# Kernel optimization log

Hardware: AMD Instinct MI355X
Metric: run time of the kernel (lower is better)

The kernel has to match this reference:

```python
import jax, jax.numpy as jnp
import numpy as np
from jax import lax

B, CHI, CHO, H, W = 8, 128, 128, 64, 64
K = 3
KK = K * K


def setup_inputs() -> dict:
    key = jax.random.key(0)
    ks = jax.random.split(key, 7)
    x = jax.random.normal(ks[0], (B, CHI, H, W), jnp.float32)
    # small offset-conv weights so sampled offsets stay in a realistic few-pixel range
    off_w = jax.random.normal(ks[1], (3 * KK, CHI, K, K), jnp.float32) * 0.01
    off_b = jnp.zeros((3 * KK,), jnp.float32)
    w = jax.random.normal(ks[2], (CHO, CHI, K, K), jnp.float32) / np.sqrt(CHI * KK).astype(np.float32)
    b = jnp.zeros((CHO,), jnp.float32)
    gamma = jax.random.uniform(ks[3], (CHO,), jnp.float32)  # nn.init.uniform_ on BN weight
    beta = jnp.zeros((CHO,), jnp.float32)
    return {"x": x, "off_w": off_w, "off_b": off_b, "w": w, "b": b, "gamma": gamma, "beta": beta}


def _deform_conv(x, off_w, off_b, w, b):
    """DCNv2 modulated deformable conv, k=3, stride=1, pad=1, dil=1, 1 deform group."""
    B_, C, H_, W_ = x.shape
    # offset/mask branch: plain 3x3 conv -> 27 channels (2*9 offsets, 9 masks)
    om = lax.conv_general_dilated(x, off_w, (1, 1), ((1, 1), (1, 1)),
                                  dimension_numbers=("NCHW", "OIHW", "NCHW"))
    om = om + off_b[None, :, None, None]
    off = om[:, : 2 * KK].reshape(B_, KK, 2, H_, W_)  # [B,9,2,H,W]; ch 2k=y, 2k+1=x
    mask = jax.nn.sigmoid(om[:, 2 * KK:])             # [B,9,H,W]

    ky, kx = jnp.meshgrid(jnp.arange(K, dtype=jnp.float32),
                          jnp.arange(K, dtype=jnp.float32), indexing="ij")
    ky = ky.reshape(KK); kx = kx.reshape(KK)
    # sampling positions: p = p0 - pad + k*dil + offset
    py = off[:, :, 0] + (jnp.arange(H_, dtype=jnp.float32) - 1.0)[None, None, :, None] + ky[None, :, None, None]
    px = off[:, :, 1] + (jnp.arange(W_, dtype=jnp.float32) - 1.0)[None, None, None, :] + kx[None, :, None, None]

    y0 = jnp.floor(py); x0 = jnp.floor(px)
    ly = py - y0; lx = px - x0
    xf = x.reshape(B_, C, H_ * W_)

    def corner(yi, xi, wgt):
        valid = ((yi >= 0) & (yi <= H_ - 1) & (xi >= 0) & (xi <= W_ - 1)).astype(x.dtype)
        yc = jnp.clip(yi, 0, H_ - 1).astype(jnp.int32)
        xc = jnp.clip(xi, 0, W_ - 1).astype(jnp.int32)
        idx = (yc * W_ + xc).reshape(B_, KK * H_ * W_)
        g = jax.vmap(lambda xb, ib: xb[:, ib])(xf, idx).reshape(B_, C, KK, H_, W_)
        return g * (valid * wgt)[:, None]

    val = (corner(y0, x0, (1 - ly) * (1 - lx))
           + corner(y0, x0 + 1, (1 - ly) * lx)
           + corner(y0 + 1, x0, ly * (1 - lx))
           + corner(y0 + 1, x0 + 1, ly * lx))  # [B,C,9,H,W]
    val = val * mask[:, None]  # modulation
    out = jnp.einsum("bckhw,ock->bohw", val, w.reshape(w.shape[0], C, KK))
    return out + b[None, :, None, None]


def reference(x, off_w, off_b, w, b, gamma, beta):
    y = _deform_conv(x, off_w, off_b, w, b)
    # BatchNorm2d in training mode (batch statistics), eps=1e-5, then ReLU
    mean = y.mean(axis=(0, 2, 3))
    var = y.var(axis=(0, 2, 3))
    yn = (y - mean[None, :, None, None]) * lax.rsqrt(var[None, :, None, None] + 1e-5)
    return jax.nn.relu(yn * gamma[None, :, None, None] + beta[None, :, None, None])
```

## Files before the change

### kernel.cpp

```cpp
#include <hip/hip_runtime.h>
#include <hip/hip_bf16.h>
#include <math.h>

#define B_ 8
#define HH 64
#define WW 64
#define HW 4096
#define LDV 136

typedef __bf16 bf16x8 __attribute__((ext_vector_type(8)));
typedef float floatx4 __attribute__((ext_vector_type(4)));
typedef unsigned int uint4a __attribute__((ext_vector_type(4)));

#define WS_Y    0u
#define WS_SC   16777216u
#define WS_SH   16778240u
#define WS_XTB  16779264u
#define WS_WTB  25167872u
#define WS_OWB  25462784u

static __device__ inline ushort f2bf(float f) {
  __hip_bfloat16 h = __float2bfloat16(f);
  return __builtin_bit_cast(ushort, h);
}
static __device__ inline float lo16(unsigned int u) { return __builtin_bit_cast(float, u << 16); }
static __device__ inline float hi16(unsigned int u) { return __builtin_bit_cast(float, u & 0xffff0000u); }

__global__ __launch_bounds__(256) void k_prepw(const float* __restrict__ w,
                                               const float* __restrict__ ow,
                                               ushort* __restrict__ wtb,
                                               ushort* __restrict__ owb) {
  int idx = blockIdx.x * 256 + threadIdx.x;
  if (idx < 147456) {
    int c = idx & 127, o = (idx >> 7) & 127, k = idx >> 14;
    wtb[idx] = f2bf(w[(o * 128 + c) * 9 + k]);
  } else {
    int j = idx - 147456;
    if (j < 36864) {
      int c = j & 127, o = (j >> 7) & 31, k = j >> 12;
      float v = (o < 27) ? ow[(o * 128 + c) * 9 + k] : 0.f;
      owb[j] = f2bf(v);
    }
  }
}

__global__ __launch_bounds__(256) void k_xt(const float* __restrict__ x,
                                            ushort* __restrict__ xtb) {
  __shared__ float tile[32][33];
  int hw0 = blockIdx.x * 32;
  int c0 = blockIdx.y * 32;
  int b = blockIdx.z;
  int col = threadIdx.x & 31, row = threadIdx.x >> 5;
  const float* xb = x + ((size_t)b * 128 + c0) * HW + hw0;
#pragma unroll
  for (int i = 0; i < 32; i += 8)
    tile[row + i][col] = xb[(size_t)(row + i) * HW + col];
  __syncthreads();
  int cpair = threadIdx.x & 15, hwi = threadIdx.x >> 4;
  ushort* xo = xtb + ((size_t)b * HW + hw0) * 128 + c0;
#pragma unroll
  for (int i = 0; i < 32; i += 16) {
    int hw = hwi + i;
    unsigned int v = (unsigned int)f2bf(tile[2 * cpair][hw]) |
                     ((unsigned int)f2bf(tile[2 * cpair + 1][hw]) << 16);
    *(unsigned int*)(&xo[(size_t)hw * 128 + 2 * cpair]) = v;
  }
}

__global__ __launch_bounds__(256) void k_main(
    const ushort* __restrict__ xtb, const ushort* __restrict__ wtb,
    const ushort* __restrict__ owb, const float* __restrict__ off_b,
    const float* __restrict__ bias, float* __restrict__ y) {
  __shared__ ushort Vl[64 * LDV];
  __shared__ float omL[27 * 64];
  int t = threadIdx.x;
  int lane = t & 63, wv = t >> 6;
  int li = lane & 15, quad = lane >> 4;
  int row = blockIdx.x, b = blockIdx.y;
  const ushort* xb = xtb + (size_t)b * HW * 128;
  int sp = lane, scg = wv;

  floatx4 oacc[2];
  oacc[0] = (floatx4){0.f, 0.f, 0.f, 0.f};
  oacc[1] = (floatx4){0.f, 0.f, 0.f, 0.f};
  for (int k = 0; k < 9; ++k) {
    int ky = k / 3, kx = k % 3;
    int ry = row - 1 + ky;
    int col = sp - 1 + kx;
    bool v = (ry >= 0 && ry < HH && col >= 0 && col < WW);
    const uint4a* src = (const uint4a*)(xb + ((size_t)(ry * WW + col) * 128 + scg * 32));
    __syncthreads();
#pragma unroll
    for (int j = 0; j < 4; ++j) {
      uint4a d = (uint4a){0u, 0u, 0u, 0u};
      if (v) d = src[j];
      *(uint4a*)(&Vl[sp * LDV + scg * 32 + j * 8]) = d;
    }
    __syncthreads();
#pragma unroll
    for (int ks = 0; ks < 4; ++ks) {
      bf16x8 bfrag = __builtin_bit_cast(bf16x8,
          *(const uint4a*)(&Vl[(wv * 16 + li) * LDV + ks * 32 + quad * 8]));
#pragma unroll
      for (int ot = 0; ot < 2; ++ot) {
        bf16x8 afrag = __builtin_bit_cast(bf16x8,
            *(const uint4a*)(&owb[(size_t)(k * 32 + ot * 16 + li) * 128 + ks * 32 + quad * 8]));
        oacc[ot] = __builtin_amdgcn_mfma_f32_16x16x32_bf16(afrag, bfrag, oacc[ot], 0, 0, 0);
      }
    }
  }
  __syncthreads();
#pragma unroll
  for (int ot = 0; ot < 2; ++ot)
#pragma unroll
    for (int r = 0; r < 4; ++r) {
      int o = ot * 16 + quad * 4 + r;
      if (o < 27) omL[o * 64 + wv * 16 + li] = oacc[ot][r] + off_b[o];
    }
  __syncthreads();

  int oh = wv & 1, ph = wv >> 1;
  floatx4 macc[4][2];
#pragma unroll
  for (int i = 0; i < 4; ++i) {
    macc[i][0] = (floatx4){0.f, 0.f, 0.f, 0.f};
    macc[i][1] = (floatx4){0.f, 0.f, 0.f, 0.f};
  }
  for (int k = 0; k < 9; ++k) {
    int ky = k / 3, kx = k % 3;
    float offy = omL[(2 * k) * 64 + sp];
    float offx = omL[(2 * k + 1) * 64 + sp];
    float mraw = omL[(18 + k) * 64 + sp];
    float m = 1.f / (1.f + __expf(-mraw));
    float py = offy + (float)(row - 1 + ky);
    float px = offx + (float)(sp - 1 + kx);
    float y0f = floorf(py), x0f = floorf(px);
    float ly = py - y0f, lx = px - x0f;
    int iy0 = (int)y0f, ix0 = (int)x0f;
    int iy1 = iy0 + 1, ix1 = ix0 + 1;
    float w00 = (1.f - ly) * (1.f - lx) * m, w01 = (1.f - ly) * lx * m;
    float w10 = ly * (1.f - lx) * m, w11 = ly * lx * m;
    if (iy0 < 0 || iy0 > HH - 1) { w00 = 0.f; w01 = 0.f; }
    if (iy1 < 0 || iy1 > HH - 1) { w10 = 0.f; w11 = 0.f; }
    if (ix0 < 0 || ix0 > WW - 1) { w00 = 0.f; w10 = 0.f; }
    if (ix1 < 0 || ix1 > WW - 1) { w01 = 0.f; w11 = 0.f; }
    int cy0 = min(max(iy0, 0), HH - 1), cy1 = min(max(iy1, 0), HH - 1);
    int cx0 = min(max(ix0, 0), WW - 1), cx1 = min(max(ix1, 0), WW - 1);
    const uint4a* r00 = (const uint4a*)(xb + ((size_t)(cy0 * WW + cx0) * 128 + scg * 32));
    const uint4a* r01 = (const uint4a*)(xb + ((size_t)(cy0 * WW + cx1) * 128 + scg * 32));
    const uint4a* r10 = (const uint4a*)(xb + ((size_t)(cy1 * WW + cx0) * 128 + scg * 32));
    const uint4a* r11 = (const uint4a*)(xb + ((size_t)(cy1 * WW + cx1) * 128 + scg * 32));
    __syncthreads();
#pragma unroll
    for (int j = 0; j < 4; ++j) {
      uint4a u00 = r00[j], u01 = r01[j], u10 = r10[j], u11 = r11[j];
      uint4a out;
#pragma unroll
      for (int e = 0; e < 4; ++e) {
        float rlo = w00 * lo16(u00[e]) + w01 * lo16(u01[e]) +
                    w10 * lo16(u10[e]) + w11 * lo16(u11[e]);
        float rhi = w00 * hi16(u00[e]) + w01 * hi16(u01[e]) +
                    w10 * hi16(u10[e]) + w11 * hi16(u11[e]);
        out[e] = (unsigned int)f2bf(rlo) | ((unsigned int)f2bf(rhi) << 16);
      }
      *(uint4a*)(&Vl[sp * LDV + scg * 32 + j * 8]) = out;
    }
    __syncthreads();
#pragma unroll
    for (int ks = 0; ks < 4; ++ks) {
      bf16x8 bf0 = __builtin_bit_cast(bf16x8,
          *(const uint4a*)(&Vl[(ph * 32 + li) * LDV + ks * 32 + quad * 8]));
      bf16x8 bf1 = __builtin_bit_cast(bf16x8,
          *(const uint4a*)(&Vl[(ph * 32 + 16 + li) * LDV + ks * 32 + quad * 8]));
#pragma unroll
      for (int ot = 0; ot < 4; ++ot) {
        bf16x8 af = __builtin_bit_cast(bf16x8,
            *(const uint4a*)(&wtb[((size_t)k * 128 + oh * 64 + ot * 16 + li) * 128 + ks * 32 + quad * 8]));
        macc[ot][0] = __builtin_amdgcn_mfma_f32_16x16x32_bf16(af, bf0, macc[ot][0], 0, 0, 0);
        macc[ot][1] = __builtin_amdgcn_mfma_f32_16x16x32_bf16(af, bf1, macc[ot][1], 0, 0, 0);
      }
    }
  }
#pragma unroll
  for (int ot = 0; ot < 4; ++ot)
#pragma unroll
    for (int pt = 0; pt < 2; ++pt)
#pragma unroll
      for (int r = 0; r < 4; ++r) {
        int o = oh * 64 + ot * 16 + quad * 4 + r;
        int p = ph * 32 + pt * 16 + li;
        float val = macc[ot][pt][r] + bias[o];
        y[((size_t)(b * 128 + o)) * HW + row * 64 + p] = val;
      }
}

__global__ __launch_bounds__(256) void k_stats(const float* __restrict__ y,
                                               const float* __restrict__ gamma,
                                               const float* __restrict__ beta,
                                               float* __restrict__ sc,
                                               float* __restrict__ sh) {
  int o = blockIdx.x, t = threadIdx.x;
  float s = 0.f, q = 0.f;
  for (int b = 0; b < 8; ++b) {
    const float4* yb = (const float4*)(y + ((size_t)(b * 128 + o)) * HW);
#pragma unroll
    for (int i = 0; i < 4; ++i) {
      float4 v = yb[t + i * 256];
      s += v.x + v.y + v.z + v.w;
      q += v.x * v.x + v.y * v.y + v.z * v.z + v.w * v.w;
    }
  }
#pragma unroll
  for (int off = 32; off >= 1; off >>= 1) {
    s += __shfl_down(s, off, 64);
    q += __shfl_down(q, off, 64);
  }
  __shared__ float bs[4], bq[4];
  if ((t & 63) == 0) { bs[t >> 6] = s; bq[t >> 6] = q; }
  __syncthreads();
  if (t == 0) {
    s = bs[0] + bs[1] + bs[2] + bs[3];
    q = bq[0] + bq[1] + bq[2] + bq[3];
    float mean = s * (1.f / 32768.f);
    float var = q * (1.f / 32768.f) - mean * mean;
    float scale = gamma[o] * rsqrtf(var + 1e-5f);
    sc[o] = scale;
    sh[o] = beta[o] - mean * scale;
  }
}

__global__ __launch_bounds__(256) void k_norm(const float* __restrict__ y,
                                              const float* __restrict__ sc,
                                              const float* __restrict__ sh,
                                              float* __restrict__ out) {
  int i4 = blockIdx.x * 256 + threadIdx.x;
  int o = (i4 >> 10) & 127;
  float scale = sc[o], shift = sh[o];
  float4 v = ((const float4*)y)[i4];
  float4 r;
  r.x = fmaxf(v.x * scale + shift, 0.f);
  r.y = fmaxf(v.y * scale + shift, 0.f);
  r.z = fmaxf(v.z * scale + shift, 0.f);
  r.w = fmaxf(v.w * scale + shift, 0.f);
  ((float4*)out)[i4] = r;
}

extern "C" void kernel_launch(void* const* d_in, const int* in_sizes, int n_in,
                              void* d_out, int out_size, void* d_ws, size_t ws_size,
                              hipStream_t stream) {
  const float* x     = (const float*)d_in[0];
  const float* off_w = (const float*)d_in[1];
  const float* off_b = (const float*)d_in[2];
  const float* w     = (const float*)d_in[3];
  const float* bias  = (const float*)d_in[4];
  const float* gamma = (const float*)d_in[5];
  const float* beta  = (const float*)d_in[6];
  float* out = (float*)d_out;
  char* ws = (char*)d_ws;

  float* y   = (float*)(ws + WS_Y);
  float* sc  = (float*)(ws + WS_SC);
  float* sh  = (float*)(ws + WS_SH);
  ushort* xtb = (ushort*)(ws + WS_XTB);
  ushort* wtb = (ushort*)(ws + WS_WTB);
  ushort* owb = (ushort*)(ws + WS_OWB);

  k_prepw<<<720, 256, 0, stream>>>(w, off_w, wtb, owb);
  k_xt<<<dim3(128, 4, 8), 256, 0, stream>>>(x, xtb);
  k_main<<<dim3(64, 8), 256, 0, stream>>>(xtb, wtb, owb, off_b, bias, y);
  k_stats<<<128, 256, 0, stream>>>(y, gamma, beta, sc, sh);
  k_norm<<<4096, 256, 0, stream>>>(y, sc, sh, out);
}
```

Measured before the change: 182.8 us.

## Split main kernel into half-row blocks with prefetched gathers and parallel stats

The main deformable-conv kernel now gives each block half a row (32 pixels) instead of a full row, doubling the grid to 1024 blocks. Each thread loads the next tap's input and bilinear corner values into registers before the current tap's MFMA step, overlapping global loads with LDS writes and compute. The batch-norm statistics kernel is spread across batch blocks and accumulates with atomics into a zeroed buffer, and scale/shift are folded into the normalize kernel. The costs are higher register pressure, recomputing the offset conv per half-row with overlapping loads, an extra memset, and atomic-order nondeterminism.

```diff
diff --git a/kernel.cpp b/kernel.cpp
--- a/kernel.cpp
+++ b/kernel.cpp
@@ -2,7 +2,6 @@
 #include <hip/hip_bf16.h>
 #include <math.h>
 
-#define B_ 8
 #define HH 64
 #define WW 64
 #define HW 4096
@@ -13,11 +12,10 @@
 typedef unsigned int uint4a __attribute__((ext_vector_type(4)));
 
 #define WS_Y    0u
-#define WS_SC   16777216u
-#define WS_SH   16778240u
-#define WS_XTB  16779264u
-#define WS_WTB  25167872u
-#define WS_OWB  25462784u
+#define WS_PSQ  16777216u
+#define WS_XTB  16778240u
+#define WS_WTB  25166848u
+#define WS_OWB  25461760u
 
 static __device__ inline ushort f2bf(float f) {
   __hip_bfloat16 h = __float2bfloat16(f);
@@ -71,69 +69,80 @@
     const ushort* __restrict__ xtb, const ushort* __restrict__ wtb,
     const ushort* __restrict__ owb, const float* __restrict__ off_b,
     const float* __restrict__ bias, float* __restrict__ y) {
-  __shared__ ushort Vl[64 * LDV];
-  __shared__ float omL[27 * 64];
+  __shared__ ushort Vl[32 * LDV];
+  __shared__ float omL[27 * 32];
   int t = threadIdx.x;
   int lane = t & 63, wv = t >> 6;
   int li = lane & 15, quad = lane >> 4;
-  int row = blockIdx.x, b = blockIdx.y;
+  int hr = blockIdx.x;
+  int row = hr >> 1, p0b = (hr & 1) * 32;
+  int b = blockIdx.y;
   const ushort* xb = xtb + (size_t)b * HW * 128;
-  int sp = lane, scg = wv;
-
-  floatx4 oacc[2];
-  oacc[0] = (floatx4){0.f, 0.f, 0.f, 0.f};
-  oacc[1] = (floatx4){0.f, 0.f, 0.f, 0.f};
+  int sp = t & 31, scg = t >> 5;
+  int gp = p0b + sp;
+
+  int mi = wv & 1, ni = wv >> 1;
+  floatx4 oacc = (floatx4){0.f, 0.f, 0.f, 0.f};
+  uint4a u0, u1;
+  {
+    int ry = row - 1, cx = gp - 1;
+    bool v = (ry >= 0 && cx >= 0);
+    int idx = v ? (ry * WW + cx) : 0;
+    const uint4a* src = (const uint4a*)(xb + (size_t)idx * 128 + scg * 16);
+    uint4a a0 = src[0], a1 = src[1];
+    u0 = v ? a0 : (uint4a){0u, 0u, 0u, 0u};
+    u1 = v ? a1 : (uint4a){0u, 0u, 0u, 0u};
+  }
   for (int k = 0; k < 9; ++k) {
-    int ky = k / 3, kx = k % 3;
-    int ry = row - 1 + ky;
-    int col = sp - 1 + kx;
-    bool v = (ry >= 0 && ry < HH && col >= 0 && col < WW);
-    const uint4a* src = (const uint4a*)(xb + ((size_t)(ry * WW + col) * 128 + scg * 32));
-    __syncthreads();
-#pragma unroll
-    for (int j = 0; j < 4; ++j) {
-      uint4a d = (uint4a){0u, 0u, 0u, 0u};
-      if (v) d = src[j];
-      *(uint4a*)(&Vl[sp * LDV + scg * 32 + j * 8]) = d;
+    __syncthreads();
+    *(uint4a*)(&Vl[sp * LDV + scg * 16]) = u0;
+    *(uint4a*)(&Vl[sp * LDV + scg * 16 + 8]) = u1;
+    if (k < 8) {
+      int kk = k + 1;
+      int ky = kk / 3, kx = kk % 3;
+      int ry = row - 1 + ky, cx = gp - 1 + kx;
+      bool v = (ry >= 0 && ry < HH && cx >= 0 && cx < WW);
+      int idx = v ? (ry * WW + cx) : 0;
+      const uint4a* src = (const uint4a*)(xb + (size_t)idx * 128 + scg * 16);
+      uint4a a0 = src[0], a1 = src[1];
+      u0 = v ? a0 : (uint4a){0u, 0u, 0u, 0u};
+      u1 = v ? a1 : (uint4a){0u, 0u, 0u, 0u};
     }
     __syncthreads();
 #pragma unroll
     for (int ks = 0; ks < 4; ++ks) {
       bf16x8 bfrag = __builtin_bit_cast(bf16x8,
-          *(const uint4a*)(&Vl[(wv * 16 + li) * LDV + ks * 32 + quad * 8]));
-#pragma unroll
-      for (int ot = 0; ot < 2; ++ot) {
-        bf16x8 afrag = __builtin_bit_cast(bf16x8,
-            *(const uint4a*)(&owb[(size_t)(k * 32 + ot * 16 + li) * 128 + ks * 32 + quad * 8]));
-        oacc[ot] = __builtin_amdgcn_mfma_f32_16x16x32_bf16(afrag, bfrag, oacc[ot], 0, 0, 0);
-      }
-    }
+          *(const uint4a*)(&Vl[(ni * 16 + li) * LDV + ks * 32 + quad * 8]));
+      bf16x8 afrag = __builtin_bit_cast(bf16x8,
+          *(const uint4a*)(&owb[(size_t)(k * 32 + mi * 16 + li) * 128 + ks * 32 + quad * 8]));
+      oacc = __builtin_amdgcn_mfma_f32_16x16x32_bf16(afrag, bfrag, oacc, 0, 0, 0);
+    }
+  }
+#pragma unroll
+  for (int r = 0; r < 4; ++r) {
+    int o = mi * 16 + quad * 4 + r;
+    if (o < 27) omL[o * 32 + ni * 16 + li] = oacc[r] + off_b[o];
   }
   __syncthreads();
-#pragma unroll
-  for (int ot = 0; ot < 2; ++ot)
-#pragma unroll
-    for (int r = 0; r < 4; ++r) {
-      int o = ot * 16 + quad * 4 + r;
-      if (o < 27) omL[o * 64 + wv * 16 + li] = oacc[ot][r] + off_b[o];
-    }
-  __syncthreads();
-
-  int oh = wv & 1, ph = wv >> 1;
-  floatx4 macc[4][2];
-#pragma unroll
-  for (int i = 0; i < 4; ++i) {
-    macc[i][0] = (floatx4){0.f, 0.f, 0.f, 0.f};
-    macc[i][1] = (floatx4){0.f, 0.f, 0.f, 0.f};
-  }
-  for (int k = 0; k < 9; ++k) {
+
+  floatx4 macc[2][2];
+#pragma unroll
+  for (int i = 0; i < 2; ++i)
+#pragma unroll
+    for (int j = 0; j < 2; ++j) macc[i][j] = (floatx4){0.f, 0.f, 0.f, 0.f};
+
+  float wq[4];
+  int idx4[4];
+  uint4a u[8];
+
+  auto prep = [&](int k) {
     int ky = k / 3, kx = k % 3;
-    float offy = omL[(2 * k) * 64 + sp];
-    float offx = omL[(2 * k + 1) * 64 + sp];
-    float mraw = omL[(18 + k) * 64 + sp];
+    float offy = omL[(2 * k) * 32 + sp];
+    float offx = omL[(2 * k + 1) * 32 + sp];
+    float mraw = omL[(18 + k) * 32 + sp];
     float m = 1.f / (1.f + __expf(-mraw));
     float py = offy + (float)(row - 1 + ky);
-    float px = offx + (float)(sp - 1 + kx);
+    float px = offx + (float)(gp - 1 + kx);
     float y0f = floorf(py), x0f = floorf(px);
     float ly = py - y0f, lx = px - x0f;
     int iy0 = (int)y0f, ix0 = (int)x0f;
@@ -146,69 +155,82 @@
     if (ix1 < 0 || ix1 > WW - 1) { w01 = 0.f; w11 = 0.f; }
     int cy0 = min(max(iy0, 0), HH - 1), cy1 = min(max(iy1, 0), HH - 1);
     int cx0 = min(max(ix0, 0), WW - 1), cx1 = min(max(ix1, 0), WW - 1);
-    const uint4a* r00 = (const uint4a*)(xb + ((size_t)(cy0 * WW + cx0) * 128 + scg * 32));
-    const uint4a* r01 = (const uint4a*)(xb + ((size_t)(cy0 * WW + cx1) * 128 + scg * 32));
-    const uint4a* r10 = (const uint4a*)(xb + ((size_t)(cy1 * WW + cx0) * 128 + scg * 32));
-    const uint4a* r11 = (const uint4a*)(xb + ((size_t)(cy1 * WW + cx1) * 128 + scg * 32));
-    __syncthreads();
-#pragma unroll
-    for (int j = 0; j < 4; ++j) {
-      uint4a u00 = r00[j], u01 = r01[j], u10 = r10[j], u11 = r11[j];
-      uint4a out;
+    idx4[0] = cy0 * WW + cx0;
+    idx4[1] = cy0 * WW + cx1;
+    idx4[2] = cy1 * WW + cx0;
+    idx4[3] = cy1 * WW + cx1;
+    wq[0] = w00; wq[1] = w01; wq[2] = w10; wq[3] = w11;
+  };
+  auto issue = [&]() {
+#pragma unroll
+    for (int c = 0; c < 4; ++c) {
+      const uint4a* s = (const uint4a*)(xb + (size_t)idx4[c] * 128 + scg * 16);
+      u[c * 2] = s[0];
+      u[c * 2 + 1] = s[1];
+    }
+  };
+
+  prep(0);
+  issue();
+  for (int k = 0; k < 9; ++k) {
+    __syncthreads();
+#pragma unroll
+    for (int j = 0; j < 2; ++j) {
+      uint4a outv;
 #pragma unroll
       for (int e = 0; e < 4; ++e) {
-        float rlo = w00 * lo16(u00[e]) + w01 * lo16(u01[e]) +
-                    w10 * lo16(u10[e]) + w11 * lo16(u11[e]);
-        float rhi = w00 * hi16(u00[e]) + w01 * hi16(u01[e]) +
-                    w10 * hi16(u10[e]) + w11 * hi16(u11[e]);
-        out[e] = (unsigned int)f2bf(rlo) | ((unsigned int)f2bf(rhi) << 16);
+        float rlo = wq[0] * lo16(u[0 + j][e]) + wq[1] * lo16(u[2 + j][e]) +
+                    wq[2] * lo16(u[4 + j][e]) + wq[3] * lo16(u[6 + j][e]);
+        float rhi = wq[0] * hi16(u[0 + j][e]) + wq[1] * hi16(u[2 + j][e]) +
+                    wq[2] * hi16(u[4 + j][e]) + wq[3] * hi16(u[6 + j][e]);
+        outv[e] = (unsigned int)f2bf(rlo) | ((unsigned int)f2bf(rhi) << 16);
       }
-      *(uint4a*)(&Vl[sp * LDV + scg * 32 + j * 8]) = out;
-    }
-    __syncthreads();
+      *(uint4a*)(&Vl[sp * LDV + scg * 16 + j * 8]) = outv;
+    }
+    if (k < 8) {
+      prep(k + 1);
+      issue();
+    }
+    __syncthreads();
+    const ushort* Arow = &wtb[(size_t)(k * 128 + wv * 32) * 128];
 #pragma unroll
     for (int ks = 0; ks < 4; ++ks) {
-      bf16x8 bf0 = __builtin_bit_cast(bf16x8,
-          *(const uint4a*)(&Vl[(ph * 32 + li) * LDV + ks * 32 + quad * 8]));
-      bf16x8 bf1 = __builtin_bit_cast(bf16x8,
-          *(const uint4a*)(&Vl[(ph * 32 + 16 + li) * LDV + ks * 32 + quad * 8]));
-#pragma unroll
-      for (int ot = 0; ot < 4; ++ot) {
-        bf16x8 af = __builtin_bit_cast(bf16x8,
-            *(const uint4a*)(&wtb[((size_t)k * 128 + oh * 64 + ot * 16 + li) * 128 + ks * 32 + quad * 8]));
-        macc[ot][0] = __builtin_amdgcn_mfma_f32_16x16x32_bf16(af, bf0, macc[ot][0], 0, 0, 0);
-        macc[ot][1] = __builtin_amdgcn_mfma_f32_16x16x32_bf16(af, bf1, macc[ot][1], 0, 0, 0);
+      bf16x8 b0 = __builtin_bit_cast(bf16x8,
+          *(const uint4a*)(&Vl[(li)*LDV + ks * 32 + quad * 8]));
+      bf16x8 b1 = __builtin_bit_cast(bf16x8,
+          *(const uint4a*)(&Vl[(16 + li) * LDV + ks * 32 + quad * 8]));
+      bf16x8 a0 = __builtin_bit_cast(bf16x8,
+          *(const uint4a*)(Arow + (size_t)(li)*128 + ks * 32 + quad * 8));
+      bf16x8 a1 = __builtin_bit_cast(bf16x8,
+          *(const uint4a*)(Arow + (size_t)(16 + li) * 128 + ks * 32 + quad * 8));
+      macc[0][0] = __builtin_amdgcn_mfma_f32_16x16x32_bf16(a0, b0, macc[0][0], 0, 0, 0);
+      macc[0][1] = __builtin_amdgcn_mfma_f32_16x16x32_bf16(a0, b1, macc[0][1], 0, 0, 0);
+      macc[1][0] = __builtin_amdgcn_mfma_f32_16x16x32_bf16(a1, b0, macc[1][0], 0, 0, 0);
+      macc[1][1] = __builtin_amdgcn_mfma_f32_16x16x32_bf16(a1, b1, macc[1][1], 0, 0, 0);
+    }
+  }
+#pragma unroll
+  for (int ot = 0; ot < 2; ++ot)
+#pragma unroll
+    for (int pt = 0; pt < 2; ++pt)
+#pragma unroll
+      for (int r = 0; r < 4; ++r) {
+        int o = wv * 32 + ot * 16 + quad * 4 + r;
+        int p = p0b + pt * 16 + li;
+        y[((size_t)(b * 128 + o)) * HW + row * 64 + p] = macc[ot][pt][r] + bias[o];
       }
-    }
-  }
-#pragma unroll
-  for (int ot = 0; ot < 4; ++ot)
-#pragma unroll
-    for (int pt = 0; pt < 2; ++pt)
-#pragma unroll
-      for (int r = 0; r < 4; ++r) {
-        int o = oh * 64 + ot * 16 + quad * 4 + r;
-        int p = ph * 32 + pt * 16 + li;
-        float val = macc[ot][pt][r] + bias[o];
-        y[((size_t)(b * 128 + o)) * HW + row * 64 + p] = val;
-      }
 }
 
 __global__ __launch_bounds__(256) void k_stats(const float* __restrict__ y,
-                                               const float* __restrict__ gamma,
-                                               const float* __restrict__ beta,
-                                               float* __restrict__ sc,
-                                               float* __restrict__ sh) {
-  int o = blockIdx.x, t = threadIdx.x;
+                                               float* __restrict__ psq) {
+  int o = blockIdx.x, b = blockIdx.y, t = threadIdx.x;
+  const float4* yb = (const float4*)(y + ((size_t)(b * 128 + o)) * HW);
   float s = 0.f, q = 0.f;
-  for (int b = 0; b < 8; ++b) {
-    const float4* yb = (const float4*)(y + ((size_t)(b * 128 + o)) * HW);
-#pragma unroll
-    for (int i = 0; i < 4; ++i) {
-      float4 v = yb[t + i * 256];
-      s += v.x + v.y + v.z + v.w;
-      q += v.x * v.x + v.y * v.y + v.z * v.z + v.w * v.w;
-    }
+#pragma unroll
+  for (int i = 0; i < 4; ++i) {
+    float4 v = yb[t + i * 256];
+    s += v.x + v.y + v.z + v.w;
+    q += v.x * v.x + v.y * v.y + v.z * v.z + v.w * v.w;
   }
 #pragma unroll
   for (int off = 32; off >= 1; off >>= 1) {
@@ -219,23 +241,24 @@
   if ((t & 63) == 0) { bs[t >> 6] = s; bq[t >> 6] = q; }
   __syncthreads();
   if (t == 0) {
-    s = bs[0] + bs[1] + bs[2] + bs[3];
-    q = bq[0] + bq[1] + bq[2] + bq[3];
-    float mean = s * (1.f / 32768.f);
-    float var = q * (1.f / 32768.f) - mean * mean;
-    float scale = gamma[o] * rsqrtf(var + 1e-5f);
-    sc[o] = scale;
-    sh[o] = beta[o] - mean * scale;
+    atomicAdd(&psq[o], bs[0] + bs[1] + bs[2] + bs[3]);
+    atomicAdd(&psq[128 + o], bq[0] + bq[1] + bq[2] + bq[3]);
   }
 }
 
 __global__ __launch_bounds__(256) void k_norm(const float* __restrict__ y,
-                                              const float* __restrict__ sc,
-                                              const float* __restrict__ sh,
+                                              const float* __restrict__ psq,
+                                              const float* __restrict__ gamma,
+                                              const float* __restrict__ beta,
                                               float* __restrict__ out) {
-  int i4 = blockIdx.x * 256 + threadIdx.x;
-  int o = (i4 >> 10) & 127;
-  float scale = sc[o], shift = sh[o];
+  int blk = blockIdx.x;
+  int o = (blk >> 2) & 127;
+  float s = psq[o], q = psq[128 + o];
+  float mean = s * (1.f / 32768.f);
+  float var = q * (1.f / 32768.f) - mean * mean;
+  float scale = gamma[o] * rsqrtf(var + 1e-5f);
+  float shift = beta[o] - mean * scale;
+  int i4 = blk * 256 + threadIdx.x;
   float4 v = ((const float4*)y)[i4];
   float4 r;
   r.x = fmaxf(v.x * scale + shift, 0.f);
@@ -258,16 +281,16 @@
   float* out = (float*)d_out;
   char* ws = (char*)d_ws;
 
-  float* y   = (float*)(ws + WS_Y);
-  float* sc  = (float*)(ws + WS_SC);
-  float* sh  = (float*)(ws + WS_SH);
+  float* y    = (float*)(ws + WS_Y);
+  float* psq  = (float*)(ws + WS_PSQ);
   ushort* xtb = (ushort*)(ws + WS_XTB);
   ushort* wtb = (ushort*)(ws + WS_WTB);
   ushort* owb = (ushort*)(ws + WS_OWB);
 
+  hipMemsetAsync(psq, 0, 256 * sizeof(float), stream);
   k_prepw<<<720, 256, 0, stream>>>(w, off_w, wtb, owb);
   k_xt<<<dim3(128, 4, 8), 256, 0, stream>>>(x, xtb);
-  k_main<<<dim3(64, 8), 256, 0, stream>>>(xtb, wtb, owb, off_b, bias, y);
-  k_stats<<<128, 256, 0, stream>>>(y, gamma, beta, sc, sh);
-  k_norm<<<4096, 256, 0, stream>>>(y, sc, sh, out);
-}
+  k_main<<<dim3(128, 8), 256, 0, stream>>>(xtb, wtb, owb, off_b, bias, y);
+  k_stats<<<dim3(128, 8), 256, 0, stream>>>(y, psq);
+  k_norm<<<4096, 256, 0, stream>>>(y, psq, gamma, beta, out);
+}
```

New measurement: 185.1 us. Within noise of the previous version (+1.2%).
